# Kernel tuning notes

Hardware: AMD Instinct MI355X
Metric: run time of the kernel (lower is better)

The kernel has to match this reference:

```python
import jax, jax.numpy as jnp
import numpy as np

M, K, L, C = 8, 4, 2, 128
C_v = C // M


def _bilinear(img, gx, gy):
    # img: [N, C_v, h, w]; gx, gy: [N, K, H, W] normalized grid coords in [-1, 1]
    # torch F.grid_sample(mode='bilinear', padding_mode='zeros', align_corners=False)
    N, Cc, h, w = img.shape
    ix = ((gx + 1.0) * w - 1.0) * 0.5
    iy = ((gy + 1.0) * h - 1.0) * 0.5
    x0 = jnp.floor(ix)
    y0 = jnp.floor(iy)
    wx1 = ix - x0
    wy1 = iy - y0
    wx0 = 1.0 - wx1
    wy0 = 1.0 - wy1

    def gather(xs, ys):
        valid = ((xs >= 0) & (xs < w) & (ys >= 0) & (ys < h)).astype(img.dtype)
        xc = jnp.clip(xs, 0, w - 1).astype(jnp.int32)
        yc = jnp.clip(ys, 0, h - 1).astype(jnp.int32)
        v = jax.vmap(lambda im, y, x: im[:, y, x])(img, yc, xc)  # [N, C_v, K, H, W]
        return v * valid[:, None]

    out = (gather(x0, y0) * (wx0 * wy0)[:, None]
           + gather(x0 + 1.0, y0) * (wx1 * wy0)[:, None]
           + gather(x0, y0 + 1.0) * (wx0 * wy1)[:, None]
           + gather(x0 + 1.0, y0 + 1.0) * (wx1 * wy1)[:, None])
    return out  # [N, C_v, K, H, W]


def _forward(z_q, x0, x1, p_q, Wq, bq, Wd, bd, Wa, ba, Wp, bp, Wm, bm):
    B, H, W, _ = z_q.shape
    zq = z_q @ Wq + bq
    # sampling offsets and attention weights
    deltas = (zq @ Wd + bd).reshape(B, H, W, M, L, K, 2)
    A = jax.nn.softmax((zq @ Wa + ba).reshape(B, H, W, M, L * K), axis=-1)
    # deltas -> [B*M, L, K, H, W, 2]; A -> [B*M, H*W, L*K]
    d = jnp.transpose(deltas, (0, 3, 4, 5, 1, 2, 6)).reshape(B * M, L, K, H, W, 2)
    An = jnp.transpose(A, (0, 3, 1, 2, 4)).reshape(B * M, H * W, L * K)
    pq = jax.lax.stop_gradient(p_q)  # phi() detaches p_q in the original

    samples = []
    for l, xl in enumerate([x0, x1]):
        h, w = xl.shape[1], xl.shape[2]
        phi = pq * jnp.array([w - 1.0, h - 1.0], dtype=z_q.dtype)  # phi(w,h,p_q)
        # NOTE: torch .repeat(M,1,1,1) tiles batch as m*B+b (replicated faithfully)
        phi = jnp.tile(phi, (M, 1, 1, 1))  # [M*B, H, W, 2]
        Wx = (xl @ Wp + bp).reshape(B, h, w, M, C_v)
        Wx = jnp.transpose(Wx, (0, 3, 4, 1, 2)).reshape(B * M, C_v, h, w)
        coords = phi[:, None] + d[:, l]  # [B*M, K, H, W, 2]
        gx = 2.0 * coords[..., 0] / max(w - 1, 1) - 1.0
        gy = 2.0 * coords[..., 1] / max(h - 1, 1) - 1.0
        s = _bilinear(Wx, gx, gy)  # [B*M, C_v, K, H, W]
        # original stacks per-k samples at dim=3 -> [B*M, C_v, H, K, W]
        samples.append(jnp.transpose(s, (0, 1, 3, 2, 4)))
    S = jnp.stack(samples, axis=1)  # [B*M, L, C_v, H, K, W]
    # faithful to original permute(0,4,5,3,1,2).view(B*M, H*W, C_v, L*K)
    S = jnp.transpose(S, (0, 4, 5, 3, 1, 2)).reshape(B * M, H * W, C_v, L * K)
    out = jnp.einsum('nlds,nls->nld', S, An)  # [B*M, H*W, C_v]
    out = out.reshape(B, M, H, W, C_v)
    out = jnp.transpose(out, (0, 2, 3, 1, 4)).reshape(B, H, W, M * C_v)
    return out @ Wm + bm


def setup_inputs() -> dict:
    key = jax.random.key(0)
    ks = jax.random.split(key, 14)
    B, H, W = 2, 128, 128
    s = 0.02
    return {
        'z_q': jax.random.normal(ks[0], (B, H, W, C), jnp.float32),
        'x0': jax.random.normal(ks[1], (B, 64, 64, C), jnp.float32),
        'x1': jax.random.normal(ks[2], (B, 128, 128, C), jnp.float32),
        'p_q': jax.random.uniform(ks[3], (B, H, W, 2), jnp.float32),
        'Wq': jax.random.normal(ks[4], (C, C), jnp.float32) * s,
        'bq': jnp.zeros((C,), jnp.float32),
        'Wd': jax.random.normal(ks[5], (C, 2 * M * K * L), jnp.float32) * s,
        'bd': jax.random.normal(ks[6], (2 * M * K * L,), jnp.float32),
        'Wa': jax.random.normal(ks[7], (C, M * K * L), jnp.float32) * s,
        'ba': jnp.full((M * K * L,), 1.0 / (L * K), jnp.float32),
        'Wp': jax.random.normal(ks[8], (C, C), jnp.float32) * s,
        'bp': jnp.zeros((C,), jnp.float32),
        'Wm': jax.random.normal(ks[9], (C, C), jnp.float32) * s,
        'bm': jnp.zeros((C,), jnp.float32),
    }


def reference(z_q, x0, x1, p_q, Wq, bq, Wd, bd, Wa, ba, Wp, bp, Wm, bm):
    return _forward(z_q, x0, x1, p_q, Wq, bq, Wd, bd, Wa, ba, Wp, bp, Wm, bm)
```

## Files before the change

kernel.cpp:

```cpp
#include <hip/hip_runtime.h>
#include <hip/hip_bf16.h>

constexpr int CB = 2;
constexpr int CH = 128;
constexpr int CW = 128;
constexpr int CM = 8;

typedef __bf16 bf16x8 __attribute__((ext_vector_type(8)));
typedef float  f32x4  __attribute__((ext_vector_type(4)));
typedef unsigned short us8 __attribute__((ext_vector_type(8)));

__device__ __forceinline__ unsigned short f2bf(float f) {
  __hip_bfloat16 h = __float2bfloat16(f);
  return *reinterpret_cast<unsigned short*>(&h);
}
__device__ __forceinline__ float bf2f(unsigned short u) {
  __hip_bfloat16 h;
  *reinterpret_cast<unsigned short*>(&h) = u;
  return __bfloat162float(h);
}

__global__ __launch_bounds__(256) void prep_all_kernel(
    const float* __restrict__ Wq, const float* __restrict__ bq,
    const float* __restrict__ Wd, const float* __restrict__ bd,
    const float* __restrict__ Wa, const float* __restrict__ ba,
    const float* __restrict__ Wp, const float* __restrict__ Wm,
    unsigned short* __restrict__ WtDA, unsigned short* __restrict__ WtP,
    unsigned short* __restrict__ WtM, float* __restrict__ bda)
{
  const int blk = blockIdx.x, t = threadIdx.x;
  if (blk < 96) {
    const int idx = blk * 256 + t;
    const int j = idx >> 7, k = idx & 127;
    float s = 0.f;
    if (j < 128) {
      for (int i = 0; i < 128; ++i) s = fmaf(Wq[k * 128 + i], Wd[i * 128 + j], s);
    } else {
      for (int i = 0; i < 128; ++i) s = fmaf(Wq[k * 128 + i], Wa[i * 64 + (j - 128)], s);
    }
    WtDA[j * 128 + k] = f2bf(s);
  } else if (blk < 224) {
    const int idx = (blk - 96) * 256 + t;
    if (idx < 16384) {
      const int k = idx >> 7, j = idx & 127;
      WtP[j * 128 + k] = f2bf(Wp[idx]);
    } else {
      const int i2 = idx - 16384;
      const int k = i2 >> 7, j = i2 & 127;
      WtM[j * 128 + k] = f2bf(Wm[i2]);
    }
  } else {
    if (t < 192) {
      const int j = t;
      float s = (j < 128) ? bd[j] : ba[j - 128];
      if (j < 128) {
        for (int i = 0; i < 128; ++i) s = fmaf(bq[i], Wd[i * 128 + j], s);
      } else {
        for (int i = 0; i < 128; ++i) s = fmaf(bq[i], Wa[i * 64 + (j - 128)], s);
      }
      bda[j] = s;
    }
  }
}

__global__ __launch_bounds__(256) void pre_gemm_kernel(
    const float* __restrict__ z_q, const float* __restrict__ x0,
    const float* __restrict__ x1,
    const unsigned short* __restrict__ WtDA, const float* __restrict__ bda,
    const unsigned short* __restrict__ WtP,  const float* __restrict__ bp,
    float* __restrict__ dl2, float* __restrict__ Alog,
    unsigned short* __restrict__ Wx, int nZ)
{
  const int t  = threadIdx.x;
  const int w  = t >> 6;
  const int l  = t & 63;
  const int lr = l & 15;
  const int kg = l >> 4;
  const int blk = blockIdx.x;

  if (blk < nZ) {
    const int r0 = blk * 64;
    const float* Ap = z_q + (size_t)(r0 + w * 16 + lr) * 128 + kg * 8;

    f32x4 acc[12];
#pragma unroll
    for (int jt = 0; jt < 12; ++jt) acc[jt] = (f32x4){0.f, 0.f, 0.f, 0.f};

#pragma unroll
    for (int k0 = 0; k0 < 128; k0 += 32) {
      const float4 f0 = *(const float4*)(Ap + k0);
      const float4 f1 = *(const float4*)(Ap + k0 + 4);
      const float ff[8] = {f0.x, f0.y, f0.z, f0.w, f1.x, f1.y, f1.z, f1.w};
      us8 uh;
#pragma unroll
      for (int i = 0; i < 8; ++i) uh[i] = f2bf(ff[i]);
      const bf16x8 ah = __builtin_bit_cast(bf16x8, uh);

      const unsigned short* Wk = WtDA + lr * 128 + k0 + kg * 8;
#pragma unroll
      for (int jt = 0; jt < 12; ++jt) {
        const bf16x8 bh = *(const bf16x8*)(Wk + jt * 16 * 128);
        acc[jt] = __builtin_amdgcn_mfma_f32_16x16x32_bf16(ah, bh, acc[jt], 0, 0, 0);
      }
    }

    const int scol = ((lr >> 1) & 3) * 32 + ((lr >> 3) & 1) * 2 + (lr & 1);
#pragma unroll
    for (int jt = 0; jt < 8; ++jt) {
      const float bv = bda[jt * 16 + lr];
#pragma unroll
      for (int rg = 0; rg < 4; ++rg) {
        const int row = r0 + w * 16 + kg * 4 + rg;
        dl2[(size_t)row * 128 + jt * 4 + scol] = acc[jt][rg] + bv;
      }
    }
#pragma unroll
    for (int jt = 8; jt < 12; ++jt) {
      const int col = (jt - 8) * 16 + lr;
      const float bv = bda[128 + col];
#pragma unroll
      for (int rg = 0; rg < 4; ++rg) {
        const int row = r0 + w * 16 + kg * 4 + rg;
        Alog[(size_t)row * 64 + col] = acc[jt][rg] + bv;
      }
    }
  } else {
    const int r0 = (blk - nZ) * 64;
    const float* A = (r0 < 8192) ? (x0 + (size_t)r0 * 128)
                                 : (x1 + (size_t)(r0 - 8192) * 128);
    const float* Ap = A + (size_t)(w * 16 + lr) * 128 + kg * 8;

    f32x4 acc[8];
#pragma unroll
    for (int jt = 0; jt < 8; ++jt) acc[jt] = (f32x4){0.f, 0.f, 0.f, 0.f};

#pragma unroll
    for (int k0 = 0; k0 < 128; k0 += 32) {
      const float4 f0 = *(const float4*)(Ap + k0);
      const float4 f1 = *(const float4*)(Ap + k0 + 4);
      const float ff[8] = {f0.x, f0.y, f0.z, f0.w, f1.x, f1.y, f1.z, f1.w};
      us8 uh, ul;
#pragma unroll
      for (int i = 0; i < 8; ++i) {
        const unsigned short hi = f2bf(ff[i]);
        uh[i] = hi;
        ul[i] = f2bf(ff[i] - bf2f(hi));
      }
      const bf16x8 ah = __builtin_bit_cast(bf16x8, uh);
      const bf16x8 al = __builtin_bit_cast(bf16x8, ul);

      const unsigned short* Wk = WtP + lr * 128 + k0 + kg * 8;
#pragma unroll
      for (int jt = 0; jt < 8; ++jt) {
        const bf16x8 bh = *(const bf16x8*)(Wk + jt * 16 * 128);
        acc[jt] = __builtin_amdgcn_mfma_f32_16x16x32_bf16(ah, bh, acc[jt], 0, 0, 0);
        acc[jt] = __builtin_amdgcn_mfma_f32_16x16x32_bf16(al, bh, acc[jt], 0, 0, 0);
      }
    }

#pragma unroll
    for (int jt = 0; jt < 8; ++jt) {
      const int col = jt * 16 + lr;
      const float bv = bp[col];
#pragma unroll
      for (int rg = 0; rg < 4; ++rg) {
        const int row = r0 + w * 16 + kg * 4 + rg;
        Wx[(size_t)row * 128 + col] = f2bf(acc[jt][rg] + bv);
      }
    }
  }
}

__global__ __launch_bounds__(256) void final_gemm_kernel(
    const unsigned short* __restrict__ Pbf,
    const unsigned short* __restrict__ WtM,
    const float* __restrict__ bm, float* __restrict__ out)
{
  const int t  = threadIdx.x;
  const int w  = t >> 6;
  const int l  = t & 63;
  const int lr = l & 15;
  const int kg = l >> 4;
  const int r0 = blockIdx.x * 64;

  const unsigned short* Ap = Pbf + (size_t)(r0 + w * 16 + lr) * 128 + kg * 8;

  f32x4 acc[8];
#pragma unroll
  for (int jt = 0; jt < 8; ++jt) acc[jt] = (f32x4){0.f, 0.f, 0.f, 0.f};

#pragma unroll
  for (int k0 = 0; k0 < 128; k0 += 32) {
    const bf16x8 av = *(const bf16x8*)(Ap + k0);
    const unsigned short* Wk = WtM + lr * 128 + k0 + kg * 8;
#pragma unroll
    for (int jt = 0; jt < 8; ++jt) {
      const bf16x8 bh = *(const bf16x8*)(Wk + jt * 16 * 128);
      acc[jt] = __builtin_amdgcn_mfma_f32_16x16x32_bf16(av, bh, acc[jt], 0, 0, 0);
    }
  }

#pragma unroll
  for (int jt = 0; jt < 8; ++jt) {
    const int col = jt * 16 + lr;
    const float bv = bm[col];
#pragma unroll
    for (int rg = 0; rg < 4; ++rg) {
      const int row = r0 + w * 16 + kg * 4 + rg;
      out[(size_t)row * 128 + col] = acc[jt][rg] + bv;
    }
  }
}

__global__ __launch_bounds__(128) void sample_attn_kernel(
    const float* __restrict__ Alog,
    const float* __restrict__ dl2,
    const float* __restrict__ p_q,
    const unsigned short* __restrict__ Wx,
    unsigned short* __restrict__ Pbf)
{
  const int q = blockIdx.x;
  const int w = q & (CW - 1);
  const int h = (q >> 7) & (CH - 1);
  const int b = q >> 14;
  const int t = threadIdx.x;
  const int m = t >> 4;
  const int c = t & 15;

  const int kk   = h >> 5;
  const int xp   = (w >> 5) + ((h & 31) << 2);
  const int yp   = (c >> 2) + ((w & 31) << 2);
  const int lp   = (c >> 1) & 1;
  const int half = c & 1;

  const size_t qp = ((size_t)b * CH + yp) * CW + xp;
  const float2 dxy = *(const float2*)(dl2 + qp * 128 + kk * 32 + m * 4 + lp * 2);

  const int pb = (b * CM + m) % CB;
  const float2 pq2 = *(const float2*)(p_q + ((((size_t)pb * CH + yp) * CW + xp) * 2));

  const float* al = Alog + (size_t)q * 64 + m * 8;
  const float4 al0 = ((const float4*)al)[0];
  const float4 al1 = ((const float4*)al)[1];

  const int wl = lp ? 128 : 64;
  const int hl = wl;
  const int imgbase = lp ? (8192 + b * 16384) : (b * 4096);

  const float cx = pq2.x * (float)(wl - 1) + dxy.x;
  const float cy = pq2.y * (float)(hl - 1) + dxy.y;
  const float gx = 2.f * cx / (float)(wl - 1) - 1.f;
  const float gy = 2.f * cy / (float)(hl - 1) - 1.f;
  const float ix = ((gx + 1.f) * (float)wl - 1.f) * 0.5f;
  const float iy = ((gy + 1.f) * (float)hl - 1.f) * 0.5f;
  const float x0f = floorf(ix), y0f = floorf(iy);
  const float fx1 = ix - x0f, fy1 = iy - y0f;
  const float fx0 = 1.f - fx1, fy0 = 1.f - fy1;
  const int xi = (int)x0f, yi = (int)y0f;

  const float vx0 = ((unsigned)xi < (unsigned)wl) ? 1.f : 0.f;
  const float vx1 = ((unsigned)(xi + 1) < (unsigned)wl) ? 1.f : 0.f;
  const float vy0 = ((unsigned)yi < (unsigned)hl) ? 1.f : 0.f;
  const float vy1 = ((unsigned)(yi + 1) < (unsigned)hl) ? 1.f : 0.f;
  const int xc0 = min(max(xi, 0), wl - 1);
  const int xc1 = min(max(xi + 1, 0), wl - 1);
  const int yc0 = min(max(yi, 0), hl - 1);
  const int yc1 = min(max(yi + 1, 0), hl - 1);

  const unsigned short* base = Wx + (size_t)imgbase * 128 + (m * 16 + half * 8);
  const unsigned short* p00 = base + (size_t)(yc0 * wl + xc0) * 128;
  const unsigned short* p01 = base + (size_t)(yc0 * wl + xc1) * 128;
  const unsigned short* p10 = base + (size_t)(yc1 * wl + xc0) * 128;
  const unsigned short* p11 = base + (size_t)(yc1 * wl + xc1) * 128;

  const us8 g00 = *(const us8*)p00;
  const us8 g01 = *(const us8*)p01;
  const us8 g10 = *(const us8*)p10;
  const us8 g11 = *(const us8*)p11;

  float lg[8] = {al0.x, al0.y, al0.z, al0.w, al1.x, al1.y, al1.z, al1.w};
  float mx = -3.0e38f;
#pragma unroll
  for (int s = 0; s < 8; ++s) mx = fmaxf(mx, lg[s]);
  float se = 0.f;
#pragma unroll
  for (int s = 0; s < 8; ++s) { lg[s] = __expf(lg[s] - mx); se += lg[s]; }
  const float inv = 1.f / se;

  const float w00 = fy0 * fx0 * vy0 * vx0;
  const float w01 = fy0 * fx1 * vy0 * vx1;
  const float w10 = fy1 * fx0 * vy1 * vx0;
  const float w11 = fy1 * fx1 * vy1 * vx1;

  float acc[8];
#pragma unroll
  for (int s = 0; s < 8; ++s) {
    float v = w00 * bf2f(g00[s]);
    v = fmaf(w01, bf2f(g01[s]), v);
    v = fmaf(w10, bf2f(g10[s]), v);
    v = fmaf(w11, bf2f(g11[s]), v);
    acc[s] = v;
  }

  float o = 0.f;
#pragma unroll
  for (int s = 0; s < 8; ++s) o = fmaf(lg[s] * inv, acc[s], o);
  Pbf[(size_t)q * 128 + t] = f2bf(o);
}

extern "C" void kernel_launch(void* const* d_in, const int* in_sizes, int n_in,
                              void* d_out, int out_size, void* d_ws, size_t ws_size,
                              hipStream_t stream)
{
  const float* z_q = (const float*)d_in[0];
  const float* x0  = (const float*)d_in[1];
  const float* x1  = (const float*)d_in[2];
  const float* p_q = (const float*)d_in[3];
  const float* Wq  = (const float*)d_in[4];
  const float* bq  = (const float*)d_in[5];
  const float* Wd  = (const float*)d_in[6];
  const float* bd  = (const float*)d_in[7];
  const float* Wa  = (const float*)d_in[8];
  const float* ba  = (const float*)d_in[9];
  const float* Wp  = (const float*)d_in[10];
  const float* bp  = (const float*)d_in[11];
  const float* Wm  = (const float*)d_in[12];
  const float* bm  = (const float*)d_in[13];

  float* ws = (float*)d_ws;
  const int NQ = CB * CH * CW;

  unsigned short* Wts  = (unsigned short*)ws;
  unsigned short* WtDA = Wts;
  unsigned short* WtP  = Wts + 24576;
  unsigned short* WtM  = Wts + 40960;
  float* bda = ws + 28672;

  float* dl2  = ws + 28864;
  float* Alog = dl2 + 4194304;
  unsigned short* Wx  = (unsigned short*)(Alog + 2097152);
  unsigned short* Pbf = Wx + 5242880;

  prep_all_kernel<<<225, 256, 0, stream>>>(Wq, bq, Wd, bd, Wa, ba, Wp, Wm,
                                           WtDA, WtP, WtM, bda);

  const int nZ = NQ / 64;
  pre_gemm_kernel<<<nZ + 640, 256, 0, stream>>>(z_q, x0, x1, WtDA, bda,
                                                WtP, bp, dl2, Alog, Wx, nZ);

  sample_attn_kernel<<<NQ, 128, 0, stream>>>(Alog, dl2, p_q, Wx, Pbf);

  final_gemm_kernel<<<NQ / 64, 256, 0, stream>>>(Pbf, WtM, bm, (float*)d_out);
}
```

Measured before the change: 200.0 us.

## Stage GEMM operands in swizzled LDS, split columns, parallelize weight prep

The three GEMM kernels now stage the B weights and the A tile into XOR-swizzled shared memory with coalesced loads. Each row tile's output columns are split across two blocks, which doubles the grid. The weight-fold prep kernel splits the K reduction over four lanes and combines them with shuffles, bf16-to-float becomes a plain shift, and the sampling kernel remaps block order and fuses the softmax-weighted accumulation. The goal is fewer redundant strided global weight loads and better occupancy, at the cost of extra LDS traffic, syncs and re-reading of the A rows per column half.

```diff
diff --git a/kernel.cpp b/kernel.cpp
--- a/kernel.cpp
+++ b/kernel.cpp
@@ -9,15 +9,16 @@
 typedef __bf16 bf16x8 __attribute__((ext_vector_type(8)));
 typedef float  f32x4  __attribute__((ext_vector_type(4)));
 typedef unsigned short us8 __attribute__((ext_vector_type(8)));
+typedef unsigned short us4 __attribute__((ext_vector_type(4)));
 
 __device__ __forceinline__ unsigned short f2bf(float f) {
   __hip_bfloat16 h = __float2bfloat16(f);
   return *reinterpret_cast<unsigned short*>(&h);
 }
 __device__ __forceinline__ float bf2f(unsigned short u) {
-  __hip_bfloat16 h;
-  *reinterpret_cast<unsigned short*>(&h) = u;
-  return __bfloat162float(h);
+  union { unsigned int i; float f; } v;
+  v.i = ((unsigned int)u) << 16;
+  return v.f;
 }
 
 __global__ __launch_bounds__(256) void prep_all_kernel(
@@ -29,38 +30,67 @@
     unsigned short* __restrict__ WtM, float* __restrict__ bda)
 {
   const int blk = blockIdx.x, t = threadIdx.x;
-  if (blk < 96) {
-    const int idx = blk * 256 + t;
+  if (blk < 384) {
+    const int gtid = blk * 256 + t;
+    const int idx = gtid >> 2;
+    const int kc  = gtid & 3;
     const int j = idx >> 7, k = idx & 127;
+    const int i0 = kc * 32;
     float s = 0.f;
     if (j < 128) {
-      for (int i = 0; i < 128; ++i) s = fmaf(Wq[k * 128 + i], Wd[i * 128 + j], s);
+#pragma unroll
+      for (int i = 0; i < 32; ++i)
+        s = fmaf(Wq[k * 128 + i0 + i], Wd[(i0 + i) * 128 + j], s);
     } else {
-      for (int i = 0; i < 128; ++i) s = fmaf(Wq[k * 128 + i], Wa[i * 64 + (j - 128)], s);
-    }
-    WtDA[j * 128 + k] = f2bf(s);
-  } else if (blk < 224) {
-    const int idx = (blk - 96) * 256 + t;
-    if (idx < 16384) {
+#pragma unroll
+      for (int i = 0; i < 32; ++i)
+        s = fmaf(Wq[k * 128 + i0 + i], Wa[(i0 + i) * 64 + (j - 128)], s);
+    }
+    s += __shfl_xor(s, 1);
+    s += __shfl_xor(s, 2);
+    if (kc == 0) WtDA[j * 128 + k] = f2bf(s);
+  } else if (blk < 448) {
+    int idx = (blk - 384) * 256 + t;
+    {
       const int k = idx >> 7, j = idx & 127;
       WtP[j * 128 + k] = f2bf(Wp[idx]);
-    } else {
-      const int i2 = idx - 16384;
-      const int k = i2 >> 7, j = i2 & 127;
-      WtM[j * 128 + k] = f2bf(Wm[i2]);
+    }
+    {
+      const int k = idx >> 7, j = idx & 127;
+      WtM[j * 128 + k] = f2bf(Wm[idx]);
     }
   } else {
     if (t < 192) {
       const int j = t;
       float s = (j < 128) ? bd[j] : ba[j - 128];
       if (j < 128) {
+#pragma unroll 8
         for (int i = 0; i < 128; ++i) s = fmaf(bq[i], Wd[i * 128 + j], s);
       } else {
+#pragma unroll 8
         for (int i = 0; i < 128; ++i) s = fmaf(bq[i], Wa[i * 64 + (j - 128)], s);
       }
       bda[j] = s;
     }
   }
+}
+
+__device__ __forceinline__ void stage_B(const unsigned short* __restrict__ src,
+                                        unsigned short* __restrict__ lds,
+                                        int n_us8)
+{
+  for (int v = threadIdx.x; v < n_us8; v += 256) {
+    const us8 d = *(const us8*)(src + v * 8);
+    const int col = v >> 4;
+    const int slot = (v & 15) ^ (col & 7);
+    *(us8*)(lds + col * 128 + slot * 8) = d;
+  }
+}
+__device__ __forceinline__ bf16x8 lds_frag(const unsigned short* __restrict__ lds,
+                                           int rc, int ko)
+{
+  const int slot = (ko >> 3) ^ (rc & 7);
+  return *(const bf16x8*)(lds + rc * 128 + slot * 8);
 }
 
 __global__ __launch_bounds__(256) void pre_gemm_kernel(
@@ -69,8 +99,10 @@
     const unsigned short* __restrict__ WtDA, const float* __restrict__ bda,
     const unsigned short* __restrict__ WtP,  const float* __restrict__ bp,
     float* __restrict__ dl2, float* __restrict__ Alog,
-    unsigned short* __restrict__ Wx, int nZ)
-{
+    unsigned short* __restrict__ Wx, int nZv)
+{
+  __shared__ __align__(16) unsigned short smem[24576];
+
   const int t  = threadIdx.x;
   const int w  = t >> 6;
   const int l  = t & 63;
@@ -78,94 +110,126 @@
   const int kg = l >> 4;
   const int blk = blockIdx.x;
 
-  if (blk < nZ) {
-    const int r0 = blk * 64;
-    const float* Ap = z_q + (size_t)(r0 + w * 16 + lr) * 128 + kg * 8;
-
-    f32x4 acc[12];
-#pragma unroll
-    for (int jt = 0; jt < 12; ++jt) acc[jt] = (f32x4){0.f, 0.f, 0.f, 0.f};
-
+  if (blk < nZv) {
+    unsigned short* Bsh = smem;
+    unsigned short* Ahi = smem + 12288;
+    const int r0 = (blk >> 1) * 64;
+    const int cg = blk & 1;
+
+    stage_B(WtDA + cg * 96 * 128, Bsh, 1536);
+    {
+      const float4* Ag = (const float4*)(z_q + (size_t)r0 * 128);
+#pragma unroll
+      for (int i = 0; i < 8; ++i) {
+        const int v = t + i * 256;
+        const float4 f = Ag[v];
+        const int flat = v * 4;
+        const int row = flat >> 7;
+        const int ko  = flat & 127;
+        us4 h;
+        h[0] = f2bf(f.x); h[1] = f2bf(f.y); h[2] = f2bf(f.z); h[3] = f2bf(f.w);
+        *(us4*)(Ahi + row * 128 + (((ko >> 3) ^ (row & 7)) << 3) + (ko & 7)) = h;
+      }
+    }
+    __syncthreads();
+
+    f32x4 acc[6];
+#pragma unroll
+    for (int jt = 0; jt < 6; ++jt) acc[jt] = (f32x4){0.f, 0.f, 0.f, 0.f};
+
+    const int lrow = w * 16 + lr;
 #pragma unroll
     for (int k0 = 0; k0 < 128; k0 += 32) {
-      const float4 f0 = *(const float4*)(Ap + k0);
-      const float4 f1 = *(const float4*)(Ap + k0 + 4);
-      const float ff[8] = {f0.x, f0.y, f0.z, f0.w, f1.x, f1.y, f1.z, f1.w};
-      us8 uh;
-#pragma unroll
-      for (int i = 0; i < 8; ++i) uh[i] = f2bf(ff[i]);
-      const bf16x8 ah = __builtin_bit_cast(bf16x8, uh);
-
-      const unsigned short* Wk = WtDA + lr * 128 + k0 + kg * 8;
-#pragma unroll
-      for (int jt = 0; jt < 12; ++jt) {
-        const bf16x8 bh = *(const bf16x8*)(Wk + jt * 16 * 128);
+      const int ko = k0 + kg * 8;
+      const bf16x8 ah = lds_frag(Ahi, lrow, ko);
+#pragma unroll
+      for (int jt = 0; jt < 6; ++jt) {
+        const bf16x8 bh = lds_frag(Bsh, jt * 16 + lr, ko);
         acc[jt] = __builtin_amdgcn_mfma_f32_16x16x32_bf16(ah, bh, acc[jt], 0, 0, 0);
       }
     }
 
     const int scol = ((lr >> 1) & 3) * 32 + ((lr >> 3) & 1) * 2 + (lr & 1);
 #pragma unroll
-    for (int jt = 0; jt < 8; ++jt) {
-      const float bv = bda[jt * 16 + lr];
-#pragma unroll
-      for (int rg = 0; rg < 4; ++rg) {
-        const int row = r0 + w * 16 + kg * 4 + rg;
-        dl2[(size_t)row * 128 + jt * 4 + scol] = acc[jt][rg] + bv;
-      }
-    }
-#pragma unroll
-    for (int jt = 8; jt < 12; ++jt) {
-      const int col = (jt - 8) * 16 + lr;
-      const float bv = bda[128 + col];
-#pragma unroll
-      for (int rg = 0; rg < 4; ++rg) {
-        const int row = r0 + w * 16 + kg * 4 + rg;
-        Alog[(size_t)row * 64 + col] = acc[jt][rg] + bv;
+    for (int jt = 0; jt < 6; ++jt) {
+      const int jtg = cg * 6 + jt;
+      if (jtg < 8) {
+        const float bv = bda[jtg * 16 + lr];
+#pragma unroll
+        for (int ri = 0; ri < 4; ++ri) {
+          const int row = r0 + w * 16 + kg * 4 + ri;
+          dl2[(size_t)row * 128 + jtg * 4 + scol] = acc[jt][ri] + bv;
+        }
+      } else {
+        const int col = (jtg - 8) * 16 + lr;
+        const float bv = bda[128 + col];
+#pragma unroll
+        for (int ri = 0; ri < 4; ++ri) {
+          const int row = r0 + w * 16 + kg * 4 + ri;
+          Alog[(size_t)row * 64 + col] = acc[jt][ri] + bv;
+        }
       }
     }
   } else {
-    const int r0 = (blk - nZ) * 64;
+    unsigned short* Bsh = smem;
+    unsigned short* Ahi = smem + 8192;
+    unsigned short* Alo = smem + 16384;
+    const int i = blk - nZv;
+    const int r0 = (i >> 1) * 64;
+    const int cg = i & 1;
     const float* A = (r0 < 8192) ? (x0 + (size_t)r0 * 128)
                                  : (x1 + (size_t)(r0 - 8192) * 128);
-    const float* Ap = A + (size_t)(w * 16 + lr) * 128 + kg * 8;
-
-    f32x4 acc[8];
-#pragma unroll
-    for (int jt = 0; jt < 8; ++jt) acc[jt] = (f32x4){0.f, 0.f, 0.f, 0.f};
-
+
+    stage_B(WtP + cg * 64 * 128, Bsh, 1024);
+    {
+      const float4* Ag = (const float4*)A;
+#pragma unroll
+      for (int ii = 0; ii < 8; ++ii) {
+        const int v = t + ii * 256;
+        const float4 f = Ag[v];
+        const int flat = v * 4;
+        const int row = flat >> 7;
+        const int ko  = flat & 127;
+        const float ff[4] = {f.x, f.y, f.z, f.w};
+        us4 h, lo;
+#pragma unroll
+        for (int u = 0; u < 4; ++u) {
+          h[u]  = f2bf(ff[u]);
+          lo[u] = f2bf(ff[u] - bf2f(h[u]));
+        }
+        const int off = row * 128 + (((ko >> 3) ^ (row & 7)) << 3) + (ko & 7);
+        *(us4*)(Ahi + off) = h;
+        *(us4*)(Alo + off) = lo;
+      }
+    }
+    __syncthreads();
+
+    f32x4 acc[4];
+#pragma unroll
+    for (int jt = 0; jt < 4; ++jt) acc[jt] = (f32x4){0.f, 0.f, 0.f, 0.f};
+
+    const int lrow = w * 16 + lr;
 #pragma unroll
     for (int k0 = 0; k0 < 128; k0 += 32) {
-      const float4 f0 = *(const float4*)(Ap + k0);
-      const float4 f1 = *(const float4*)(Ap + k0 + 4);
-      const float ff[8] = {f0.x, f0.y, f0.z, f0.w, f1.x, f1.y, f1.z, f1.w};
-      us8 uh, ul;
-#pragma unroll
-      for (int i = 0; i < 8; ++i) {
-        const unsigned short hi = f2bf(ff[i]);
-        uh[i] = hi;
-        ul[i] = f2bf(ff[i] - bf2f(hi));
-      }
-      const bf16x8 ah = __builtin_bit_cast(bf16x8, uh);
-      const bf16x8 al = __builtin_bit_cast(bf16x8, ul);
-
-      const unsigned short* Wk = WtP + lr * 128 + k0 + kg * 8;
-#pragma unroll
-      for (int jt = 0; jt < 8; ++jt) {
-        const bf16x8 bh = *(const bf16x8*)(Wk + jt * 16 * 128);
+      const int ko = k0 + kg * 8;
+      const bf16x8 ah = lds_frag(Ahi, lrow, ko);
+      const bf16x8 al = lds_frag(Alo, lrow, ko);
+#pragma unroll
+      for (int jt = 0; jt < 4; ++jt) {
+        const bf16x8 bh = lds_frag(Bsh, jt * 16 + lr, ko);
         acc[jt] = __builtin_amdgcn_mfma_f32_16x16x32_bf16(ah, bh, acc[jt], 0, 0, 0);
         acc[jt] = __builtin_amdgcn_mfma_f32_16x16x32_bf16(al, bh, acc[jt], 0, 0, 0);
       }
     }
 
 #pragma unroll
-    for (int jt = 0; jt < 8; ++jt) {
-      const int col = jt * 16 + lr;
+    for (int jt = 0; jt < 4; ++jt) {
+      const int col = cg * 64 + jt * 16 + lr;
       const float bv = bp[col];
 #pragma unroll
-      for (int rg = 0; rg < 4; ++rg) {
-        const int row = r0 + w * 16 + kg * 4 + rg;
-        Wx[(size_t)row * 128 + col] = f2bf(acc[jt][rg] + bv);
+      for (int ri = 0; ri < 4; ++ri) {
+        const int row = r0 + w * 16 + kg * 4 + ri;
+        Wx[(size_t)row * 128 + col] = f2bf(acc[jt][ri] + bv);
       }
     }
   }
@@ -176,38 +240,46 @@
     const unsigned short* __restrict__ WtM,
     const float* __restrict__ bm, float* __restrict__ out)
 {
+  __shared__ __align__(16) unsigned short smem[16384];
+  unsigned short* Bsh = smem;
+  unsigned short* Ash = smem + 8192;
+
   const int t  = threadIdx.x;
   const int w  = t >> 6;
   const int l  = t & 63;
   const int lr = l & 15;
   const int kg = l >> 4;
-  const int r0 = blockIdx.x * 64;
-
-  const unsigned short* Ap = Pbf + (size_t)(r0 + w * 16 + lr) * 128 + kg * 8;
-
-  f32x4 acc[8];
-#pragma unroll
-  for (int jt = 0; jt < 8; ++jt) acc[jt] = (f32x4){0.f, 0.f, 0.f, 0.f};
-
+  const int r0 = (blockIdx.x >> 1) * 64;
+  const int cg = blockIdx.x & 1;
+
+  stage_B(WtM + cg * 64 * 128, Bsh, 1024);
+  stage_B(Pbf + (size_t)r0 * 128, Ash, 1024);
+  __syncthreads();
+
+  f32x4 acc[4];
+#pragma unroll
+  for (int jt = 0; jt < 4; ++jt) acc[jt] = (f32x4){0.f, 0.f, 0.f, 0.f};
+
+  const int lrow = w * 16 + lr;
 #pragma unroll
   for (int k0 = 0; k0 < 128; k0 += 32) {
-    const bf16x8 av = *(const bf16x8*)(Ap + k0);
-    const unsigned short* Wk = WtM + lr * 128 + k0 + kg * 8;
-#pragma unroll
-    for (int jt = 0; jt < 8; ++jt) {
-      const bf16x8 bh = *(const bf16x8*)(Wk + jt * 16 * 128);
+    const int ko = k0 + kg * 8;
+    const bf16x8 av = lds_frag(Ash, lrow, ko);
+#pragma unroll
+    for (int jt = 0; jt < 4; ++jt) {
+      const bf16x8 bh = lds_frag(Bsh, jt * 16 + lr, ko);
       acc[jt] = __builtin_amdgcn_mfma_f32_16x16x32_bf16(av, bh, acc[jt], 0, 0, 0);
     }
   }
 
 #pragma unroll
-  for (int jt = 0; jt < 8; ++jt) {
-    const int col = jt * 16 + lr;
+  for (int jt = 0; jt < 4; ++jt) {
+    const int col = cg * 64 + jt * 16 + lr;
     const float bv = bm[col];
 #pragma unroll
-    for (int rg = 0; rg < 4; ++rg) {
-      const int row = r0 + w * 16 + kg * 4 + rg;
-      out[(size_t)row * 128 + col] = acc[jt][rg] + bv;
+    for (int ri = 0; ri < 4; ++ri) {
+      const int row = r0 + w * 16 + kg * 4 + ri;
+      out[(size_t)row * 128 + col] = acc[jt][ri] + bv;
     }
   }
 }
@@ -219,7 +291,8 @@
     const unsigned short* __restrict__ Wx,
     unsigned short* __restrict__ Pbf)
 {
-  const int q = blockIdx.x;
+  const int bid = blockIdx.x;
+  const int q = (bid & 7) * 4096 + (bid >> 3);
   const int w = q & (CW - 1);
   const int h = (q >> 7) & (CH - 1);
   const int b = q >> 14;
@@ -292,19 +365,15 @@
   const float w10 = fy1 * fx0 * vy1 * vx0;
   const float w11 = fy1 * fx1 * vy1 * vx1;
 
-  float acc[8];
+  float o = 0.f;
 #pragma unroll
   for (int s = 0; s < 8; ++s) {
     float v = w00 * bf2f(g00[s]);
     v = fmaf(w01, bf2f(g01[s]), v);
     v = fmaf(w10, bf2f(g10[s]), v);
     v = fmaf(w11, bf2f(g11[s]), v);
-    acc[s] = v;
-  }
-
-  float o = 0.f;
-#pragma unroll
-  for (int s = 0; s < 8; ++s) o = fmaf(lg[s] * inv, acc[s], o);
+    o = fmaf(lg[s] * inv, v, o);
+  }
   Pbf[(size_t)q * 128 + t] = f2bf(o);
 }
 
@@ -341,14 +410,14 @@
   unsigned short* Wx  = (unsigned short*)(Alog + 2097152);
   unsigned short* Pbf = Wx + 5242880;
 
-  prep_all_kernel<<<225, 256, 0, stream>>>(Wq, bq, Wd, bd, Wa, ba, Wp, Wm,
+  prep_all_kernel<<<449, 256, 0, stream>>>(Wq, bq, Wd, bd, Wa, ba, Wp, Wm,
                                            WtDA, WtP, WtM, bda);
 
-  const int nZ = NQ / 64;
-  pre_gemm_kernel<<<nZ + 640, 256, 0, stream>>>(z_q, x0, x1, WtDA, bda,
-                                                WtP, bp, dl2, Alog, Wx, nZ);
+  const int nZv = 1024;
+  pre_gemm_kernel<<<nZv + 1280, 256, 0, stream>>>(z_q, x0, x1, WtDA, bda,
+                                                  WtP, bp, dl2, Alog, Wx, nZv);
 
   sample_attn_kernel<<<NQ, 128, 0, stream>>>(Alog, dl2, p_q, Wx, Pbf);
 
-  final_gemm_kernel<<<NQ / 64, 256, 0, stream>>>(Pbf, WtM, bm, (float*)d_out);
-}
+  final_gemm_kernel<<<NQ / 32, 256, 0, stream>>>(Pbf, WtM, bm, (float*)d_out);
+}
```

Result: faster. 182.8 us (-8.6%).
